# Kernel tuning notes

Measured on AMD Instinct MI355X. Metric: run time of the kernel, lower is better.

## Reference

```python
import jax, jax.numpy as jnp
import numpy as np

N = 100000
E = 1600000
D_IN = 128
K = 2
D_OUT = 128


def setup_inputs() -> dict:
    key = jax.random.key(0)
    k1, k2, k3, k4, k5, k6 = jax.random.split(key, 6)
    x = jax.random.normal(k1, (N, D_IN), dtype=jnp.float32)
    edge_src = jax.random.randint(k2, (E,), 0, N, dtype=jnp.int32)  # row indices of sparse adj
    edge_dst = jax.random.randint(k3, (E,), 0, N, dtype=jnp.int32)  # col indices of sparse adj
    edge_val = jax.random.uniform(k4, (E,), dtype=jnp.float32)
    # Linear(in_features*(k+1), out_features), xavier_normal with relu gain
    fan_in = D_IN * (K + 1)
    gain = np.sqrt(2.0)  # calculate_gain('relu')
    std = gain * np.sqrt(2.0 / (fan_in + D_OUT))
    W = jax.random.normal(k5, (D_OUT, fan_in), dtype=jnp.float32) * std
    b = jax.random.uniform(k6, (D_OUT,), dtype=jnp.float32, minval=-1.0, maxval=1.0) / np.sqrt(fan_in)
    return {"x": x, "edge_src": edge_src, "edge_dst": edge_dst, "edge_val": edge_val, "W": W, "b": b}


def _spmm(edge_src, edge_dst, edge_val, feat):
    # y[i] = sum_{e: src[e]==i} val[e] * feat[dst[e]]
    msgs = edge_val[:, None] * feat[edge_dst]  # [E, D]
    return jax.ops.segment_sum(msgs, edge_src, num_segments=N)


def reference(x, edge_src, edge_dst, edge_val, W, b):
    fstack = [x]
    for _ in range(K):
        fstack.append(_spmm(edge_src, edge_dst, edge_val, fstack[-1]))
    h = jnp.concatenate(fstack, axis=-1)  # [N, D_IN*(K+1)]
    out = h @ W.T + b  # [N, D_OUT]
    # norm=False, activation=None, dropout=False per init defaults
    return out
```

## Files before the change

### kernel.cpp

```cpp
#include <hip/hip_runtime.h>
#include <hip/hip_bf16.h>

#define NN 100000
#define EE 1600000
#define D 128
#define BKT 391
#define CAP 5120

typedef __attribute__((ext_vector_type(4))) float f32x4;
typedef __attribute__((ext_vector_type(8))) short s16x8;

__device__ inline ushort f2bf(float f) {
    uint b = __float_as_uint(f);
    return (ushort)((b + 0x7fffu + ((b >> 16) & 1u)) >> 16);
}
__device__ inline float bflo(uint g) { return __uint_as_float(g << 16); }
__device__ inline float bfhi(uint g) { return __uint_as_float(g & 0xffff0000u); }

__global__ __launch_bounds__(256) void cvt_bf16(
    const float* __restrict__ in, ushort* __restrict__ out, int n4)
{
    const int i = blockIdx.x * 256 + threadIdx.x;
    if (i >= n4) return;
    const float4 v = reinterpret_cast<const float4*>(in)[i];
    ushort4 o;
    o.x = f2bf(v.x); o.y = f2bf(v.y); o.z = f2bf(v.z); o.w = f2bf(v.w);
    reinterpret_cast<ushort4*>(out)[i] = o;
}

__global__ __launch_bounds__(256) void bucket_pass1(
    const int* __restrict__ src, const int* __restrict__ dst,
    const float* __restrict__ val, int* __restrict__ cursor,
    int2* __restrict__ barr)
{
    __shared__ int cnt[BKT];
    __shared__ int basel[BKT];
    const int t = threadIdx.x;
    for (int u = t; u < BKT; u += 256) cnt[u] = 0;
    __syncthreads();

    int eb[8], elr[8], ew1[8], ev[8];
    const int e0 = blockIdx.x * 2048 + t;
    #pragma unroll
    for (int it = 0; it < 8; ++it) {
        const int e = e0 + it * 256;
        eb[it] = -1;
        if (e < EE) {
            const int s = src[e];
            const int bk = s >> 8;
            eb[it]  = bk;
            elr[it] = atomicAdd(&cnt[bk], 1);
            ew1[it] = dst[e] | ((s & 255) << 17);
            ev[it]  = __float_as_int(val[e]);
        }
    }
    __syncthreads();
    for (int u = t; u < BKT; u += 256)
        basel[u] = (cnt[u] > 0) ? atomicAdd(&cursor[u], cnt[u]) : 0;
    __syncthreads();
    #pragma unroll
    for (int it = 0; it < 8; ++it) {
        if (eb[it] >= 0)
            barr[(size_t)eb[it] * CAP + basel[eb[it]] + elr[it]] =
                make_int2(ev[it], ew1[it]);
    }
}

__global__ __launch_bounds__(512) void scan_buckets(
    const int* __restrict__ cursor, int* __restrict__ bbase, int* __restrict__ rp)
{
    __shared__ int tmp[512];
    const int t = threadIdx.x;
    const int s = (t < BKT) ? cursor[t] : 0;
    tmp[t] = s;
    __syncthreads();
    for (int off = 1; off < 512; off <<= 1) {
        const int v = (t >= off) ? tmp[t - off] : 0;
        __syncthreads();
        tmp[t] += v;
        __syncthreads();
    }
    if (t < BKT) bbase[t] = tmp[t] - s;
    if (t == BKT - 1) bbase[BKT] = tmp[t];
    if (t == 0) rp[NN] = EE;
}

__global__ __launch_bounds__(256) void bucket_pass2(
    const int* __restrict__ bbase, const int2* __restrict__ barr,
    int* __restrict__ rp, int2* __restrict__ csr)
{
    __shared__ int rowcnt[256];
    __shared__ int tmp[256];
    __shared__ int rowoff[256];
    __shared__ ushort lrk[CAP];
    const int b = blockIdx.x;
    const int t = threadIdx.x;
    const int gbase = bbase[b];
    const int sz    = bbase[b + 1] - gbase;
    const int2* my  = barr + (size_t)b * CAP;

    rowcnt[t] = 0;
    __syncthreads();
    for (int i = t; i < sz; i += 256) {
        const int rl = (my[i].y >> 17) & 255;
        lrk[i] = (ushort)atomicAdd(&rowcnt[rl], 1);
    }
    __syncthreads();
    const int c = rowcnt[t];
    tmp[t] = c;
    __syncthreads();
    for (int off = 1; off < 256; off <<= 1) {
        const int v = (t >= off) ? tmp[t - off] : 0;
        __syncthreads();
        tmp[t] += v;
        __syncthreads();
    }
    rowoff[t] = tmp[t] - c;
    const int row = b * 256 + t;
    if (row < NN) rp[row] = gbase + (tmp[t] - c);
    __syncthreads();
    for (int i = t; i < sz; i += 256) {
        const int2 e = my[i];
        const int rl = (e.y >> 17) & 255;
        csr[gbase + rowoff[rl] + lrk[i]] = make_int2(e.y & 0x1FFFF, e.x);
    }
}

__global__ __launch_bounds__(256) void spmm_csr_bf16(
    const int* __restrict__ rp, const int2* __restrict__ csr,
    const ushort* __restrict__ featb, ushort* __restrict__ outb)
{
    const int tid  = blockIdx.x * 256 + threadIdx.x;
    const int row  = tid >> 6;
    const int lane = threadIdx.x & 63;
    const int g    = lane >> 4;
    const int li   = lane & 15;

    const int start = rp[row];
    const int end   = rp[row + 1];

    float acc[8] = {0.f, 0.f, 0.f, 0.f, 0.f, 0.f, 0.f, 0.f};

    for (int base = start; base < end; base += 8) {
        const int p0 = base + g;
        const int p1 = base + 4 + g;
        int2 e0 = make_int2(0, 0), e1 = make_int2(0, 0);
        if (p0 < end) e0 = csr[p0];
        if (p1 < end) e1 = csr[p1];
        const float v0 = __int_as_float(e0.y);
        const float v1 = __int_as_float(e1.y);
        const uint4 g0 = *reinterpret_cast<const uint4*>(featb + (size_t)e0.x * 128 + li * 8);
        const uint4 g1 = *reinterpret_cast<const uint4*>(featb + (size_t)e1.x * 128 + li * 8);
        acc[0] = fmaf(v0, bflo(g0.x), acc[0]); acc[1] = fmaf(v0, bfhi(g0.x), acc[1]);
        acc[2] = fmaf(v0, bflo(g0.y), acc[2]); acc[3] = fmaf(v0, bfhi(g0.y), acc[3]);
        acc[4] = fmaf(v0, bflo(g0.z), acc[4]); acc[5] = fmaf(v0, bfhi(g0.z), acc[5]);
        acc[6] = fmaf(v0, bflo(g0.w), acc[6]); acc[7] = fmaf(v0, bfhi(g0.w), acc[7]);
        acc[0] = fmaf(v1, bflo(g1.x), acc[0]); acc[1] = fmaf(v1, bfhi(g1.x), acc[1]);
        acc[2] = fmaf(v1, bflo(g1.y), acc[2]); acc[3] = fmaf(v1, bfhi(g1.y), acc[3]);
        acc[4] = fmaf(v1, bflo(g1.z), acc[4]); acc[5] = fmaf(v1, bfhi(g1.z), acc[5]);
        acc[6] = fmaf(v1, bflo(g1.w), acc[6]); acc[7] = fmaf(v1, bfhi(g1.w), acc[7]);
    }

    #pragma unroll
    for (int i = 0; i < 8; ++i) {
        acc[i] += __shfl_xor(acc[i], 16);
        acc[i] += __shfl_xor(acc[i], 32);
    }

    if (g == 0) {
        uint4 o;
        o.x = ((uint)f2bf(acc[1]) << 16) | (uint)f2bf(acc[0]);
        o.y = ((uint)f2bf(acc[3]) << 16) | (uint)f2bf(acc[2]);
        o.z = ((uint)f2bf(acc[5]) << 16) | (uint)f2bf(acc[4]);
        o.w = ((uint)f2bf(acc[7]) << 16) | (uint)f2bf(acc[6]);
        *reinterpret_cast<uint4*>(outb + (size_t)row * 128 + li * 8) = o;
    }
}

__global__ __launch_bounds__(512) void gemm_mfma(
    const ushort* __restrict__ xb, const ushort* __restrict__ f1b,
    const ushort* __restrict__ f2b, const ushort* __restrict__ Wb,
    const float* __restrict__ b, float* __restrict__ out)
{
    __shared__ ushort Ws[128 * 64];

    const int t    = threadIdx.x;
    const int wave = t >> 6;
    const int lane = t & 63;
    const int lr   = lane & 15;
    const int lg   = lane >> 4;
    const int rbase = blockIdx.x * 128;

    int arow = rbase + wave * 16 + lr;
    if (arow >= NN) arow = NN - 1;

    f32x4 acc[8];
    #pragma unroll
    for (int j = 0; j < 8; ++j) {
        const float bv = b[j * 16 + lr];
        acc[j] = (f32x4){bv, bv, bv, bv};
    }

    for (int c = 0; c < 6; ++c) {
        const ushort* src = (c < 2) ? xb : ((c < 4) ? f1b : f2b);
        const int col0 = (c & 1) * 64;
        const int k0w  = c * 64;

        #pragma unroll
        for (int it = 0; it < 2; ++it) {
            const int idx = it * 512 + t;
            const int col = idx >> 3, seg = idx & 7;
            const s16x8 v = *reinterpret_cast<const s16x8*>(Wb + (size_t)col * 384 + k0w + seg * 8);
            *reinterpret_cast<s16x8*>(&Ws[col * 64 + ((seg ^ (col & 7)) * 8)]) = v;
        }

        const s16x8 a0 = *reinterpret_cast<const s16x8*>(src + (size_t)arow * 128 + col0 + lg * 8);
        const s16x8 a1 = *reinterpret_cast<const s16x8*>(src + (size_t)arow * 128 + col0 + 32 + lg * 8);

        __syncthreads();

        #pragma unroll
        for (int kk = 0; kk < 2; ++kk) {
            const s16x8 a = kk ? a1 : a0;
            #pragma unroll
            for (int j = 0; j < 8; ++j) {
                const int bcol = j * 16 + lr;
                const int bch  = (kk * 4 + lg) ^ (bcol & 7);
                const s16x8 bf = *reinterpret_cast<const s16x8*>(&Ws[bcol * 64 + bch * 8]);
                acc[j] = __builtin_amdgcn_mfma_f32_16x16x32_bf16(a, bf, acc[j], 0, 0, 0);
            }
        }
        __syncthreads();
    }

    #pragma unroll
    for (int j = 0; j < 8; ++j) {
        #pragma unroll
        for (int j2 = 0; j2 < 4; ++j2) {
            const int rg = rbase + wave * 16 + lg * 4 + j2;
            if (rg < NN)
                out[(size_t)rg * 128 + j * 16 + lr] = acc[j][j2];
        }
    }
}

extern "C" void kernel_launch(void* const* d_in, const int* in_sizes, int n_in,
                              void* d_out, int out_size, void* d_ws, size_t ws_size,
                              hipStream_t stream)
{
    const float* x    = (const float*)d_in[0];
    const int*   esrc = (const int*)  d_in[1];
    const int*   edst = (const int*)  d_in[2];
    const float* eval = (const float*)d_in[3];
    const float* W    = (const float*)d_in[4];
    const float* b    = (const float*)d_in[5];
    float* out = (float*)d_out;

    char* ws = (char*)d_ws;
    const size_t FB = (size_t)NN * D * 2;
    ushort* xb     = (ushort*)(ws);
    ushort* f1b    = (ushort*)(ws + FB);
    ushort* f2b    = (ushort*)(ws + 2 * FB);
    ushort* Wb     = (ushort*)(ws + 3 * FB);
    char*   p      = ws + 3 * FB + 98304;
    int2*   csr    = (int2*)p;               p += (size_t)EE * 8;
    int2*   barr   = (int2*)p;               p += (size_t)BKT * CAP * 8;
    int*    cursor = (int*)p;                p += (BKT + 1) * 4;
    int*    bbase  = (int*)p;                p += (BKT + 1) * 4;
    int*    rp     = (int*)p;

    hipMemsetAsync(cursor, 0, BKT * sizeof(int), stream);

    cvt_bf16<<<(NN * D / 4 + 255) / 256, 256, 0, stream>>>(x, xb, NN * D / 4);
    cvt_bf16<<<(128 * 384 / 4 + 255) / 256, 256, 0, stream>>>(W, Wb, 128 * 384 / 4);

    bucket_pass1<<<(EE + 2047) / 2048, 256, 0, stream>>>(esrc, edst, eval, cursor, barr);
    scan_buckets<<<1, 512, 0, stream>>>(cursor, bbase, rp);
    bucket_pass2<<<BKT, 256, 0, stream>>>(bbase, barr, rp, csr);

    spmm_csr_bf16<<<NN / 4, 256, 0, stream>>>(rp, csr, xb,  f1b);
    spmm_csr_bf16<<<NN / 4, 256, 0, stream>>>(rp, csr, f1b, f2b);

    gemm_mfma<<<(NN + 127) / 128, 512, 0, stream>>>(xb, f1b, f2b, Wb, b, out);
}
```

Measured before the change: 323.3 us.

## Stage bucket and CSR scatters in LDS and widen SpMM gather unroll

Result: faster. 315.8 us (-2.3%).

```diff
diff --git a/kernel.cpp b/kernel.cpp
--- a/kernel.cpp
+++ b/kernel.cpp
@@ -33,36 +33,67 @@
     const float* __restrict__ val, int* __restrict__ cursor,
     int2* __restrict__ barr)
 {
-    __shared__ int cnt[BKT];
-    __shared__ int basel[BKT];
+    __shared__ int    cnt[BKT];
+    __shared__ int    lbase[BKT];
+    __shared__ int    gbase[BKT];
+    __shared__ int    tmp[256];
+    __shared__ int2   staged[2048];
+    __shared__ ushort bkt_of[2048];
     const int t = threadIdx.x;
     for (int u = t; u < BKT; u += 256) cnt[u] = 0;
     __syncthreads();
 
-    int eb[8], elr[8], ew1[8], ev[8];
+    int ebk[8], erk[8]; int2 epk[8];
     const int e0 = blockIdx.x * 2048 + t;
     #pragma unroll
     for (int it = 0; it < 8; ++it) {
         const int e = e0 + it * 256;
-        eb[it] = -1;
+        ebk[it] = -1;
         if (e < EE) {
             const int s = src[e];
             const int bk = s >> 8;
-            eb[it]  = bk;
-            elr[it] = atomicAdd(&cnt[bk], 1);
-            ew1[it] = dst[e] | ((s & 255) << 17);
-            ev[it]  = __float_as_int(val[e]);
-        }
-    }
-    __syncthreads();
+            ebk[it] = bk;
+            erk[it] = atomicAdd(&cnt[bk], 1);
+            epk[it] = make_int2(__float_as_int(val[e]), dst[e] | ((s & 255) << 17));
+        }
+    }
+    __syncthreads();
+
+    {
+        const int i0 = 2 * t, i1 = 2 * t + 1;
+        const int c0 = (i0 < BKT) ? cnt[i0] : 0;
+        const int c1 = (i1 < BKT) ? cnt[i1] : 0;
+        const int s = c0 + c1;
+        tmp[t] = s;
+        __syncthreads();
+        for (int off = 1; off < 256; off <<= 1) {
+            const int v = (t >= off) ? tmp[t - off] : 0;
+            __syncthreads();
+            tmp[t] += v;
+            __syncthreads();
+        }
+        const int excl = tmp[t] - s;
+        if (i0 < BKT) lbase[i0] = excl;
+        if (i1 < BKT) lbase[i1] = excl + c0;
+    }
     for (int u = t; u < BKT; u += 256)
-        basel[u] = (cnt[u] > 0) ? atomicAdd(&cursor[u], cnt[u]) : 0;
-    __syncthreads();
+        gbase[u] = (cnt[u] > 0) ? atomicAdd(&cursor[u], cnt[u]) : 0;
+    __syncthreads();
+
     #pragma unroll
     for (int it = 0; it < 8; ++it) {
-        if (eb[it] >= 0)
-            barr[(size_t)eb[it] * CAP + basel[eb[it]] + elr[it]] =
-                make_int2(ev[it], ew1[it]);
+        if (ebk[it] >= 0) {
+            const int pos = lbase[ebk[it]] + erk[it];
+            staged[pos] = epk[it];
+            bkt_of[pos] = (ushort)ebk[it];
+        }
+    }
+    __syncthreads();
+
+    const int total = min(2048, EE - blockIdx.x * 2048);
+    for (int i = t; i < total; i += 256) {
+        const int bk = bkt_of[i];
+        barr[(size_t)bk * CAP + gbase[bk] + (i - lbase[bk])] = staged[i];
     }
 }
 
@@ -91,20 +122,18 @@
 {
     __shared__ int rowcnt[256];
     __shared__ int tmp[256];
-    __shared__ int rowoff[256];
-    __shared__ ushort lrk[CAP];
+    __shared__ int rowcur[256];
+    __shared__ int2 sorted[CAP];
     const int b = blockIdx.x;
     const int t = threadIdx.x;
-    const int gbase = bbase[b];
-    const int sz    = bbase[b + 1] - gbase;
-    const int2* my  = barr + (size_t)b * CAP;
+    const int gb = bbase[b];
+    const int sz = bbase[b + 1] - gb;
+    const int2* my = barr + (size_t)b * CAP;
 
     rowcnt[t] = 0;
     __syncthreads();
-    for (int i = t; i < sz; i += 256) {
-        const int rl = (my[i].y >> 17) & 255;
-        lrk[i] = (ushort)atomicAdd(&rowcnt[rl], 1);
-    }
+    for (int i = t; i < sz; i += 256)
+        atomicAdd(&rowcnt[(my[i].y >> 17) & 255], 1);
     __syncthreads();
     const int c = rowcnt[t];
     tmp[t] = c;
@@ -115,15 +144,20 @@
         tmp[t] += v;
         __syncthreads();
     }
-    rowoff[t] = tmp[t] - c;
+    const int excl = tmp[t] - c;
+    rowcur[t] = excl;
     const int row = b * 256 + t;
-    if (row < NN) rp[row] = gbase + (tmp[t] - c);
+    if (row < NN) rp[row] = gb + excl;
     __syncthreads();
     for (int i = t; i < sz; i += 256) {
         const int2 e = my[i];
         const int rl = (e.y >> 17) & 255;
-        csr[gbase + rowoff[rl] + lrk[i]] = make_int2(e.y & 0x1FFFF, e.x);
-    }
+        const int slot = atomicAdd(&rowcur[rl], 1);
+        sorted[slot] = make_int2(e.y & 0x1FFFF, e.x);
+    }
+    __syncthreads();
+    for (int i = t; i < sz; i += 256)
+        csr[gb + i] = sorted[i];
 }
 
 __global__ __launch_bounds__(256) void spmm_csr_bf16(
@@ -141,24 +175,19 @@
 
     float acc[8] = {0.f, 0.f, 0.f, 0.f, 0.f, 0.f, 0.f, 0.f};
 
-    for (int base = start; base < end; base += 8) {
-        const int p0 = base + g;
-        const int p1 = base + 4 + g;
-        int2 e0 = make_int2(0, 0), e1 = make_int2(0, 0);
-        if (p0 < end) e0 = csr[p0];
-        if (p1 < end) e1 = csr[p1];
-        const float v0 = __int_as_float(e0.y);
-        const float v1 = __int_as_float(e1.y);
-        const uint4 g0 = *reinterpret_cast<const uint4*>(featb + (size_t)e0.x * 128 + li * 8);
-        const uint4 g1 = *reinterpret_cast<const uint4*>(featb + (size_t)e1.x * 128 + li * 8);
-        acc[0] = fmaf(v0, bflo(g0.x), acc[0]); acc[1] = fmaf(v0, bfhi(g0.x), acc[1]);
-        acc[2] = fmaf(v0, bflo(g0.y), acc[2]); acc[3] = fmaf(v0, bfhi(g0.y), acc[3]);
-        acc[4] = fmaf(v0, bflo(g0.z), acc[4]); acc[5] = fmaf(v0, bfhi(g0.z), acc[5]);
-        acc[6] = fmaf(v0, bflo(g0.w), acc[6]); acc[7] = fmaf(v0, bfhi(g0.w), acc[7]);
-        acc[0] = fmaf(v1, bflo(g1.x), acc[0]); acc[1] = fmaf(v1, bfhi(g1.x), acc[1]);
-        acc[2] = fmaf(v1, bflo(g1.y), acc[2]); acc[3] = fmaf(v1, bfhi(g1.y), acc[3]);
-        acc[4] = fmaf(v1, bflo(g1.z), acc[4]); acc[5] = fmaf(v1, bfhi(g1.z), acc[5]);
-        acc[6] = fmaf(v1, bflo(g1.w), acc[6]); acc[7] = fmaf(v1, bfhi(g1.w), acc[7]);
+    for (int base = start; base < end; base += 16) {
+        #pragma unroll
+        for (int k = 0; k < 4; ++k) {
+            const int p  = base + k * 4 + g;
+            const int pc = (p < end) ? p : start;
+            const int2 e = csr[pc];
+            const float v = (p < end) ? __int_as_float(e.y) : 0.f;
+            const uint4 gg = *reinterpret_cast<const uint4*>(featb + (size_t)e.x * 128 + li * 8);
+            acc[0] = fmaf(v, bflo(gg.x), acc[0]); acc[1] = fmaf(v, bfhi(gg.x), acc[1]);
+            acc[2] = fmaf(v, bflo(gg.y), acc[2]); acc[3] = fmaf(v, bfhi(gg.y), acc[3]);
+            acc[4] = fmaf(v, bflo(gg.z), acc[4]); acc[5] = fmaf(v, bfhi(gg.z), acc[5]);
+            acc[6] = fmaf(v, bflo(gg.w), acc[6]); acc[7] = fmaf(v, bfhi(gg.w), acc[7]);
+        }
     }
 
     #pragma unroll
```
